# Kernel tuning notes

Measured on AMD Instinct MI355X. Metric: run time of the kernel, lower is better.

Reference implementation:

```python
import jax, jax.numpy as jnp
import numpy as np

B, C, H, W = 8, 512, 64, 64
R = 16
CQK = C // R  # 32


def setup_inputs() -> dict:
    key = jax.random.key(0)
    kx, kq, kk, kv = jax.random.split(key, 4)
    x = jax.random.normal(kx, (B, C, H, W), dtype=jnp.float32)
    # Conv1d with kernel_size=1, bias=False == matmul over channel dim
    Wq = jax.random.normal(kq, (CQK, C), dtype=jnp.float32) * (1.0 / np.sqrt(C))
    Wk = jax.random.normal(kk, (CQK, C), dtype=jnp.float32) * (1.0 / np.sqrt(C))
    Wv = jax.random.normal(kv, (C, C), dtype=jnp.float32) * (1.0 / np.sqrt(C))
    return {"x": x, "Wq": Wq, "Wk": Wk, "Wv": Wv}


def reference(x, Wq, Wk, Wv):
    b, c, h, w = x.shape
    xf = x.reshape(b, c, h * w)                 # [b, c, n]
    q = jnp.einsum('dc,bcn->bdn', Wq, xf)       # [b, c/r, n]
    k = jnp.einsum('dc,bcn->bdn', Wk, xf)       # [b, c/r, n]
    attn = jax.nn.softmax(jnp.einsum('bdm,bdn->bmn', q, k), axis=-1)  # [b, n, n]
    v = jnp.einsum('dc,bcn->bdn', Wv, xf)       # [b, c, n]
    out = jnp.einsum('bcm,bmn->bcn', v, attn)   # [b, c, n]
    return out.reshape(b, c, h, w)
```

## Files before the change

### kernel.cpp

```cpp
#include <hip/hip_runtime.h>
#include <hip/hip_bf16.h>


typedef __attribute__((ext_vector_type(8))) short s16x8;
typedef __attribute__((ext_vector_type(4))) float f32x4;

#define MFMA16(a, b, c) __builtin_amdgcn_mfma_f32_16x16x32_bf16((a), (b), (c), 0, 0, 0)

__device__ __forceinline__ ushort f2bf(float f) {
  union { float f; unsigned u; } v; v.f = f;
  return (ushort)((v.u + 0x8000u) >> 16);
}
__device__ __forceinline__ unsigned pack_bf16(float lo, float hi) {
  union { float f; unsigned u; } a, b; a.f = lo; b.f = hi;
  return __builtin_amdgcn_perm(b.u + 0x8000u, a.u + 0x8000u, 0x07060302u);
}
__device__ __forceinline__ float fexp2(float x) { return __builtin_amdgcn_exp2f(x); }

__device__ __forceinline__ void chunk_barrier() {
  asm volatile("s_waitcnt lgkmcnt(0)" ::: "memory");
  __builtin_amdgcn_s_barrier();
  __builtin_amdgcn_sched_barrier(0);
}

__global__ void k_cvt_w(const float* __restrict__ Wq, const float* __restrict__ Wk,
                        const float* __restrict__ Wv, ushort* __restrict__ Wqb,
                        ushort* __restrict__ Wkb, ushort* __restrict__ Wvb) {
  int i = blockIdx.x * 256 + threadIdx.x;
  if (i < 262144) Wvb[i] = f2bf(Wv[i]);
  else if (i < 278528) Wqb[i - 262144] = f2bf(Wq[i - 262144] * 1.4426950408889634f);
  else if (i < 294912) Wkb[i - 278528] = f2bf(Wk[i - 278528]);
}

__global__ __launch_bounds__(256) void k_xpose(const float* __restrict__ x,
                                               ushort* __restrict__ xT) {
  const int b = blockIdx.z, c0 = blockIdx.y * 64, n0 = blockIdx.x * 256;
  __shared__ uint U[2][64][65];
  const int t = threadIdx.x;
  const int wv = t >> 6, ln = t & 63;
  const float* xp = x + ((size_t)b * 512 + c0 + wv * 16) * 4096 + n0 + ln * 4;
#pragma unroll
  for (int i = 0; i < 16; ++i) {
    float4 f = *(const float4*)(xp + (size_t)i * 4096);
    U[0][wv * 16 + i][ln] = pack_bf16(f.x, f.y);
    U[1][wv * 16 + i][ln] = pack_bf16(f.z, f.w);
  }
  __syncthreads();
  const int c_seg = (t & 7) * 8;
#pragma unroll
  for (int pass = 0; pass < 8; ++pass) {
    const int nl = pass * 32 + (t >> 3);
    const int p = nl >> 1;
    const int h = p & 1, idx = p >> 1;
    const uint sel = (nl & 1) ? 0x07060302u : 0x05040100u;
    uint o[4];
#pragma unroll
    for (int j = 0; j < 4; ++j) {
      uint ua = U[h][c_seg + 2 * j][idx];
      uint ub = U[h][c_seg + 2 * j + 1][idx];
      o[j] = __builtin_amdgcn_perm(ub, ua, sel);
    }
    *(uint4*)(xT + ((size_t)b * 4096 + n0 + nl) * 512 + c0 + c_seg) = *(uint4*)o;
  }
}

__global__ __launch_bounds__(256, 2) void k_proj(const ushort* __restrict__ xT,
                                                 const ushort* __restrict__ Wqb,
                                                 const ushort* __restrict__ Wkb,
                                                 const ushort* __restrict__ Wvb,
                                                 ushort* __restrict__ qb,
                                                 ushort* __restrict__ kb,
                                                 ushort* __restrict__ vb) {
  const int b = blockIdx.y, n0 = blockIdx.x * 64;
  const int lane = threadIdx.x & 63, w = threadIdx.x >> 6;
  const int quad = lane >> 4, l15 = lane & 15;
  const ushort* xT_b = xT + (size_t)b * 4096 * 512;

  const ushort* Wqk = (w < 2) ? (Wqb + (size_t)(w * 16 + l15) * 512)
                              : (Wkb + (size_t)((w - 2) * 16 + l15) * 512);

  f32x4 accv[8][4], accqk[4];
#pragma unroll
  for (int i = 0; i < 8; ++i)
#pragma unroll
    for (int nt = 0; nt < 4; ++nt) accv[i][nt] = {0.f, 0.f, 0.f, 0.f};
#pragma unroll
  for (int nt = 0; nt < 4; ++nt) accqk[nt] = {0.f, 0.f, 0.f, 0.f};

  for (int k0 = 0; k0 < 512; k0 += 32) {
    s16x8 bx[4];
#pragma unroll
    for (int nt = 0; nt < 4; ++nt)
      bx[nt] = *(const s16x8*)(xT_b + (size_t)(n0 + nt * 16 + l15) * 512 + k0 + quad * 8);
#pragma unroll
    for (int i = 0; i < 8; ++i) {
      s16x8 av = *(const s16x8*)(Wvb + (size_t)((8 * w + i) * 16 + l15) * 512 + k0 + quad * 8);
#pragma unroll
      for (int nt = 0; nt < 4; ++nt) accv[i][nt] = MFMA16(av, bx[nt], accv[i][nt]);
    }
    s16x8 aqk = *(const s16x8*)(Wqk + k0 + quad * 8);
#pragma unroll
    for (int nt = 0; nt < 4; ++nt) accqk[nt] = MFMA16(aqk, bx[nt], accqk[nt]);
  }

  ushort* vb_b = vb + (size_t)b * 512 * 4096;
#pragma unroll
  for (int i = 0; i < 8; ++i)
#pragma unroll
    for (int nt = 0; nt < 4; ++nt)
#pragma unroll
      for (int r = 0; r < 4; ++r)
        vb_b[(size_t)((8 * w + i) * 16 + quad * 4 + r) * 4096 + n0 + nt * 16 + l15] =
            f2bf(accv[i][nt][r]);

  ushort* qk_out = (w < 2) ? (qb + (size_t)b * 4096 * 32) : (kb + (size_t)b * 4096 * 32);
#pragma unroll
  for (int nt = 0; nt < 4; ++nt) {
    ushort4 u;
    u.x = f2bf(accqk[nt][0]); u.y = f2bf(accqk[nt][1]);
    u.z = f2bf(accqk[nt][2]); u.w = f2bf(accqk[nt][3]);
    *(ushort4*)(qk_out + (size_t)(n0 + nt * 16 + l15) * 32 + (w & 1) * 16 + quad * 4) = u;
  }
}

__global__ __launch_bounds__(256) void k_pass1(const ushort* __restrict__ qb,
                                               const ushort* __restrict__ kb,
                                               float* __restrict__ Lneg) {
  const int b = blockIdx.y, mt = blockIdx.x;
  const int lane = threadIdx.x & 63, w = threadIdx.x >> 6;
  const int quad = lane >> 4, l15 = lane & 15;
  const int m = mt * 64 + w * 16;
  const ushort* qb_b = qb + (size_t)b * 4096 * 32;
  const ushort* kb_b = kb + (size_t)b * 4096 * 32;
  const s16x8 aqf = *(const s16x8*)(qb_b + (size_t)(m + l15) * 32 + quad * 8);
  float ps[4] = {0.f, 0.f, 0.f, 0.f};
  const f32x4 zf = {0.f, 0.f, 0.f, 0.f};
  for (int n0 = 0; n0 < 4096; n0 += 64) {
#pragma unroll
    for (int nt = 0; nt < 4; ++nt) {
      s16x8 bk = *(const s16x8*)(kb_b + (size_t)(n0 + nt * 16 + l15) * 32 + quad * 8);
      f32x4 s = MFMA16(aqf, bk, zf);
#pragma unroll
      for (int r = 0; r < 4; ++r) ps[r] += fexp2(s[r]);
    }
  }
  for (int off = 1; off < 16; off <<= 1)
#pragma unroll
    for (int r = 0; r < 4; ++r) ps[r] += __shfl_xor(ps[r], off, 64);
  if (l15 == 0)
#pragma unroll
    for (int r = 0; r < 4; ++r)
      Lneg[(size_t)b * 4096 + m + quad * 4 + r] = -log2f(ps[r]);
}

__global__ __launch_bounds__(512, 2) void k_pass2(const ushort* __restrict__ qb,
                                                  const ushort* __restrict__ kb,
                                                  const ushort* __restrict__ vb,
                                                  const float* __restrict__ Lneg,
                                                  float* __restrict__ out) {
  const int blk = blockIdx.x;
  const int b = blk & 7, ntb = blk >> 3;
  const int nbase = ntb * 128;
  const int lane = threadIdx.x & 63, w = threadIdx.x >> 6;
  const int quad = lane >> 4, l15 = lane & 15;
  const int cbase = w * 64;
  const int swz = l15 & 7;
  const int Mw = w >> 1;
  const int Tb = (w & 1) * 4;

  __shared__ __align__(16) ushort PT[2][128 * 64];

  const ushort* qb_b = qb + (size_t)b * 4096 * 32;
  const ushort* kb_b = kb + (size_t)b * 4096 * 32;
  const ushort* vb_b = vb + (size_t)b * 512 * 4096;
  const float* L_b = Lneg + (size_t)b * 4096;

  s16x8 kf[4];
#pragma unroll
  for (int i = 0; i < 4; ++i)
    kf[i] = *(const s16x8*)(kb_b + (size_t)(nbase + (Tb + i) * 16 + l15) * 32 + quad * 8);

  f32x4 acc[4][8];
#pragma unroll
  for (int ci = 0; ci < 4; ++ci)
#pragma unroll
    for (int nt = 0; nt < 8; ++nt) acc[ci][nt] = {0.f, 0.f, 0.f, 0.f};

  s16x8 aqp;
  float4 l4p;
  s16x8 va0[4], va1[4];

  auto loadQ = [&](int chunk) {
    const int m0 = chunk * 64;
    aqp = *(const s16x8*)(qb_b + (size_t)(m0 + Mw * 16 + l15) * 32 + quad * 8);
    l4p = *(const float4*)(L_b + m0 + Mw * 16 + quad * 4);
  };
  auto loadV0 = [&](int chunk) {
    const int m0 = chunk * 64;
#pragma unroll
    for (int ci = 0; ci < 4; ++ci)
      va0[ci] = *(const s16x8*)(vb_b + (size_t)(cbase + ci * 16 + l15) * 4096 + m0 + quad * 8);
  };
  auto loadV1 = [&](int chunk) {
    const int m0 = chunk * 64;
#pragma unroll
    for (int ci = 0; ci < 4; ++ci)
      va1[ci] = *(const s16x8*)(vb_b + (size_t)(cbase + ci * 16 + l15) * 4096 + m0 + 32 + quad * 8);
  };
  auto produce_tile = [&](int buf, int i) {
    char* Pw = (char*)&PT[buf][0];
    const int T = Tb + i;
    f32x4 cin; cin.x = l4p.x; cin.y = l4p.y; cin.z = l4p.z; cin.w = l4p.w;
    f32x4 s = MFMA16(aqp, kf[i], cin);
    uint2 u;
    u.x = pack_bf16(fexp2(s.x), fexp2(s.y));
    u.y = pack_bf16(fexp2(s.z), fexp2(s.w));
    const int row = T * 16 + l15;
    const int gran = (2 * Mw + (quad >> 1)) ^ swz;
    *(uint2*)(Pw + row * 128 + gran * 16 + (quad & 1) * 8) = u;
  };

  loadQ(0);
#pragma unroll
  for (int i = 0; i < 4; ++i) produce_tile(0, i);
  loadQ(1);
  loadV0(0);
  loadV1(0);

  for (int chunk = 0; chunk < 64; ++chunk) {
    const int buf = chunk & 1;
    chunk_barrier();
    const char* P = (const char*)&PT[buf][0];
    s16x8 pg[8];
#pragma unroll
    for (int nt = 0; nt < 8; ++nt)
      pg[nt] = *(const s16x8*)(P + (nt * 16 + l15) * 128 + (quad ^ swz) * 16);
#pragma unroll
    for (int i = 0; i < 4; ++i) produce_tile(buf ^ 1, i);
    if (chunk < 62) loadQ(chunk + 2);
    __builtin_amdgcn_s_setprio(1);
    s16x8 rr[8];
#pragma unroll
    for (int nt = 0; nt < 8; ++nt) {
#pragma unroll
      for (int ci = 0; ci < 4; ++ci) acc[ci][nt] = MFMA16(va0[ci], pg[nt], acc[ci][nt]);
      rr[nt] = *(const s16x8*)(P + (nt * 16 + l15) * 128 + ((4 + quad) ^ swz) * 16);
    }
    __builtin_amdgcn_s_setprio(0);
    if (chunk < 63) loadV0(chunk + 1);
    __builtin_amdgcn_s_setprio(1);
#pragma unroll
    for (int nt = 0; nt < 8; ++nt)
#pragma unroll
      for (int ci = 0; ci < 4; ++ci) acc[ci][nt] = MFMA16(va1[ci], rr[nt], acc[ci][nt]);
    __builtin_amdgcn_s_setprio(0);
    if (chunk < 63) loadV1(chunk + 1);
  }

  float* out_b = out + (size_t)b * 512 * 4096;
#pragma unroll
  for (int ci = 0; ci < 4; ++ci)
#pragma unroll
    for (int nt = 0; nt < 8; ++nt) {
      const int n = nbase + nt * 16 + l15;
      const int c0 = cbase + ci * 16 + quad * 4;
#pragma unroll
      for (int r = 0; r < 4; ++r) out_b[(size_t)(c0 + r) * 4096 + n] = acc[ci][nt][r];
    }
}

extern "C" void kernel_launch(void* const* d_in, const int* in_sizes, int n_in,
                              void* d_out, int out_size, void* d_ws, size_t ws_size,
                              hipStream_t stream) {
  const float* x  = (const float*)d_in[0];
  const float* Wq = (const float*)d_in[1];
  const float* Wk = (const float*)d_in[2];
  const float* Wv = (const float*)d_in[3];
  float* out = (float*)d_out;

  char* ws = (char*)d_ws;
  ushort* vb  = (ushort*)(ws + 0);
  ushort* xT  = (ushort*)(ws + 33554432);
  ushort* qb  = (ushort*)(ws + 67108864);
  ushort* kb  = (ushort*)(ws + 69206016);
  ushort* Wvb = (ushort*)(ws + 71303168);
  ushort* Wqb = (ushort*)(ws + 71827456);
  ushort* Wkb = (ushort*)(ws + 71860224);
  float*  Lrs = (float*)(ws + 71892992);

  hipLaunchKernelGGL(k_cvt_w, dim3(1152), dim3(256), 0, stream, Wq, Wk, Wv, Wqb, Wkb, Wvb);
  hipLaunchKernelGGL(k_xpose, dim3(16, 8, 8), dim3(256), 0, stream, x, xT);
  hipLaunchKernelGGL(k_proj, dim3(64, 8), dim3(256), 0, stream, xT, Wqb, Wkb, Wvb, qb, kb, vb);
  hipLaunchKernelGGL(k_pass1, dim3(64, 8), dim3(256), 0, stream, qb, kb, Lrs);
  hipLaunchKernelGGL(k_pass2, dim3(256), dim3(512), 0, stream, qb, kb, vb, Lrs, out);
}
```

Measured before the change: 341.7 us.

## Fuse x transpose and bf16 conversion into projection kernel via LDS

```diff
diff --git a/kernel.cpp b/kernel.cpp
--- a/kernel.cpp
+++ b/kernel.cpp
@@ -32,39 +32,7 @@
   else if (i < 294912) Wkb[i - 278528] = f2bf(Wk[i - 278528]);
 }
 
-__global__ __launch_bounds__(256) void k_xpose(const float* __restrict__ x,
-                                               ushort* __restrict__ xT) {
-  const int b = blockIdx.z, c0 = blockIdx.y * 64, n0 = blockIdx.x * 256;
-  __shared__ uint U[2][64][65];
-  const int t = threadIdx.x;
-  const int wv = t >> 6, ln = t & 63;
-  const float* xp = x + ((size_t)b * 512 + c0 + wv * 16) * 4096 + n0 + ln * 4;
-#pragma unroll
-  for (int i = 0; i < 16; ++i) {
-    float4 f = *(const float4*)(xp + (size_t)i * 4096);
-    U[0][wv * 16 + i][ln] = pack_bf16(f.x, f.y);
-    U[1][wv * 16 + i][ln] = pack_bf16(f.z, f.w);
-  }
-  __syncthreads();
-  const int c_seg = (t & 7) * 8;
-#pragma unroll
-  for (int pass = 0; pass < 8; ++pass) {
-    const int nl = pass * 32 + (t >> 3);
-    const int p = nl >> 1;
-    const int h = p & 1, idx = p >> 1;
-    const uint sel = (nl & 1) ? 0x07060302u : 0x05040100u;
-    uint o[4];
-#pragma unroll
-    for (int j = 0; j < 4; ++j) {
-      uint ua = U[h][c_seg + 2 * j][idx];
-      uint ub = U[h][c_seg + 2 * j + 1][idx];
-      o[j] = __builtin_amdgcn_perm(ub, ua, sel);
-    }
-    *(uint4*)(xT + ((size_t)b * 4096 + n0 + nl) * 512 + c0 + c_seg) = *(uint4*)o;
-  }
-}
-
-__global__ __launch_bounds__(256, 2) void k_proj(const ushort* __restrict__ xT,
+__global__ __launch_bounds__(256, 2) void k_proj(const float* __restrict__ x,
                                                  const ushort* __restrict__ Wqb,
                                                  const ushort* __restrict__ Wkb,
                                                  const ushort* __restrict__ Wvb,
@@ -72,9 +40,43 @@
                                                  ushort* __restrict__ kb,
                                                  ushort* __restrict__ vb) {
   const int b = blockIdx.y, n0 = blockIdx.x * 64;
-  const int lane = threadIdx.x & 63, w = threadIdx.x >> 6;
+  const int t = threadIdx.x;
+  const int lane = t & 63, w = t >> 6;
   const int quad = lane >> 4, l15 = lane & 15;
-  const ushort* xT_b = xT + (size_t)b * 4096 * 512;
+
+  __shared__ __align__(16) ushort XB[64 * 512];
+  __shared__ uint U[2][32][17];
+
+  const float* x_b = x + (size_t)b * 512 * 4096;
+
+  for (int s = 0; s < 16; ++s) {
+    const int c0s = s * 32;
+#pragma unroll
+    for (int k = 0; k < 2; ++k) {
+      const int idx = t + k * 256;
+      const int cr = idx >> 4, c4 = idx & 15;
+      float4 f = *(const float4*)(x_b + (size_t)(c0s + cr) * 4096 + n0 + c4 * 4);
+      U[0][cr][c4] = pack_bf16(f.x, f.y);
+      U[1][cr][c4] = pack_bf16(f.z, f.w);
+    }
+    __syncthreads();
+    {
+      const int n = t & 63, gl = t >> 6;
+      const int h = (n >> 1) & 1, c4 = n >> 2;
+      const uint sel = (n & 1) ? 0x07060302u : 0x05040100u;
+      uint o[4];
+#pragma unroll
+      for (int j = 0; j < 4; ++j) {
+        uint ua = U[h][gl * 8 + 2 * j][c4];
+        uint ub = U[h][gl * 8 + 2 * j + 1][c4];
+        o[j] = __builtin_amdgcn_perm(ub, ua, sel);
+      }
+      const int gfull = (c0s >> 3) + gl;
+      const int gsw = gfull ^ (n & 7);
+      *(uint4*)((char*)XB + n * 1024 + gsw * 16) = *(uint4*)o;
+    }
+    __syncthreads();
+  }
 
   const ushort* Wqk = (w < 2) ? (Wqb + (size_t)(w * 16 + l15) * 512)
                               : (Wkb + (size_t)((w - 2) * 16 + l15) * 512);
@@ -87,11 +89,14 @@
 #pragma unroll
   for (int nt = 0; nt < 4; ++nt) accqk[nt] = {0.f, 0.f, 0.f, 0.f};
 
+  const char* XBb = (const char*)XB;
   for (int k0 = 0; k0 < 512; k0 += 32) {
     s16x8 bx[4];
 #pragma unroll
-    for (int nt = 0; nt < 4; ++nt)
-      bx[nt] = *(const s16x8*)(xT_b + (size_t)(n0 + nt * 16 + l15) * 512 + k0 + quad * 8);
+    for (int nt = 0; nt < 4; ++nt) {
+      const int nl = nt * 16 + l15;
+      bx[nt] = *(const s16x8*)(XBb + nl * 1024 + ((((k0 >> 3) + quad) ^ (nl & 7)) << 4));
+    }
 #pragma unroll
     for (int i = 0; i < 8; ++i) {
       s16x8 av = *(const s16x8*)(Wvb + (size_t)((8 * w + i) * 16 + l15) * 512 + k0 + quad * 8);
@@ -280,17 +285,15 @@
 
   char* ws = (char*)d_ws;
   ushort* vb  = (ushort*)(ws + 0);
-  ushort* xT  = (ushort*)(ws + 33554432);
-  ushort* qb  = (ushort*)(ws + 67108864);
-  ushort* kb  = (ushort*)(ws + 69206016);
-  ushort* Wvb = (ushort*)(ws + 71303168);
-  ushort* Wqb = (ushort*)(ws + 71827456);
-  ushort* Wkb = (ushort*)(ws + 71860224);
-  float*  Lrs = (float*)(ws + 71892992);
+  ushort* qb  = (ushort*)(ws + 33554432);
+  ushort* kb  = (ushort*)(ws + 35651584);
+  ushort* Wvb = (ushort*)(ws + 37748736);
+  ushort* Wqb = (ushort*)(ws + 38273024);
+  ushort* Wkb = (ushort*)(ws + 38305792);
+  float*  Lrs = (float*)(ws + 38338560);
 
   hipLaunchKernelGGL(k_cvt_w, dim3(1152), dim3(256), 0, stream, Wq, Wk, Wv, Wqb, Wkb, Wvb);
-  hipLaunchKernelGGL(k_xpose, dim3(16, 8, 8), dim3(256), 0, stream, x, xT);
-  hipLaunchKernelGGL(k_proj, dim3(64, 8), dim3(256), 0, stream, xT, Wqb, Wkb, Wvb, qb, kb, vb);
+  hipLaunchKernelGGL(k_proj, dim3(64, 8), dim3(256), 0, stream, x, Wqb, Wkb, Wvb, qb, kb, vb);
   hipLaunchKernelGGL(k_pass1, dim3(64, 8), dim3(256), 0, stream, qb, kb, Lrs);
   hipLaunchKernelGGL(k_pass2, dim3(256), dim3(512), 0, stream, qb, kb, vb, Lrs, out);
 }
```

Result: faster. 322.5 us (-5.6%).
